# Kernel optimization log

Measured on AMD Instinct MI355X. Metric: run time of the kernel, lower is better.

The kernel has to match this reference:

```python
import jax, jax.numpy as jnp
import numpy as np

N, E, H, L, B = 50000, 1250000, 64, 64, 500
BN_EPS = 1e-5


def _bn(x, g, b):
    # training-mode BatchNorm1d: per-feature batch mean / biased var
    m = jnp.mean(x, axis=0)
    v = jnp.mean((x - m) ** 2, axis=0)
    return (x - m) * jax.lax.rsqrt(v + BN_EPS) * g + b


def _gconv(h, edge_attr, src, dst):
    # message: softplus(x_j + edge_attr); aggr='add'; eps=0 -> + (1+0)*h
    msg = jax.nn.softplus(h[src] + edge_attr)          # [E,H]
    agg = jax.ops.segment_sum(msg, dst, num_segments=N)  # [N,H]
    return agg + h


def setup_inputs() -> dict:
    key = jax.random.key(0)
    ks = jax.random.split(key, 24)
    s = 0.05
    inp = {
        "x": jax.random.normal(ks[0], (E, 1), jnp.float32),
        "node_type": jax.random.randint(ks[1], (N,), 0, 100),
        "edge_type": jax.random.randint(ks[2], (E,), 0, 100),
        "edge_index": jax.random.randint(ks[3], (2, E), 0, N),
        "batch": jnp.sort(jax.random.randint(ks[4], (N,), 0, B)),
        "node_emb": jax.random.normal(ks[5], (100, H)) * s,
        "edge_emb": jax.random.normal(ks[6], (100, H)) * s,
        "w_d1": jax.random.normal(ks[7], (H, 1)) * s,
        "b_d1": jnp.zeros((H,)),
        "g_d1": jnp.ones((H,)), "be_d1": jnp.zeros((H,)),
        "w_d2": jax.random.normal(ks[8], (H, H)) * s,
        "b_d2": jnp.zeros((H,)),
        "g_d2": jnp.ones((H,)), "be_d2": jnp.zeros((H,)),
        "g_c1": jnp.ones((H,)), "be_c1": jnp.zeros((H,)),
        "g_c2": jnp.ones((H,)), "be_c2": jnp.zeros((H,)),
        "g_c3": jnp.ones((H,)), "be_c3": jnp.zeros((H,)),
        "w_o1": jax.random.normal(ks[9], (H, 2 * H)) * s,
        "b_o1": jnp.zeros((H,)),
        "g_o1": jnp.ones((H,)), "be_o1": jnp.zeros((H,)),
        "w_o2": jax.random.normal(ks[10], (H // 2, H)) * s,
        "b_o2": jnp.zeros((H // 2,)),
        "g_o2": jnp.ones((H // 2,)), "be_o2": jnp.zeros((H // 2,)),
        "w_o3": jax.random.normal(ks[11], (2 * L, H // 2)) * s,
        "b_o3": jnp.zeros((2 * L,)),
    }
    return inp


def reference(x, node_type, edge_type, edge_index, batch,
              node_emb, edge_emb,
              w_d1, b_d1, g_d1, be_d1,
              w_d2, b_d2, g_d2, be_d2,
              g_c1, be_c1, g_c2, be_c2, g_c3, be_c3,
              w_o1, b_o1, g_o1, be_o1,
              w_o2, b_o2, g_o2, be_o2,
              w_o3, b_o3):
    act = jax.nn.softplus
    src, dst = edge_index[0], edge_index[1]
    node_attr = node_emb[node_type]                    # [N,H]
    ea = edge_emb[edge_type]                           # [E,H]
    d = act(_bn(x @ w_d1.T + b_d1, g_d1, be_d1))       # [E,H]
    d = _bn(d @ w_d2.T + b_d2, g_d2, be_d2)
    ea = d * ea
    h = node_attr
    h = act(_bn(_gconv(h, ea, src, dst), g_c1, be_c1))
    h = act(_bn(_gconv(h, ea, src, dst), g_c2, be_c2))
    h = _bn(_gconv(h, ea, src, dst), g_c3, be_c3)
    h_global = jax.ops.segment_sum(h, batch, num_segments=B)  # [B,H]
    nf = jnp.concatenate([h, h_global[batch]], axis=-1)       # [N,2H]
    nf = act(_bn(nf @ w_o1.T + b_o1, g_o1, be_o1))
    nf = act(_bn(nf @ w_o2.T + b_o2, g_o2, be_o2))
    out = nf @ w_o3.T + b_o3                           # [N,2L]
    return out[:, :L], out[:, L:]
```

## Files before the change

### kernel.cpp

```cpp
#include <hip/hip_runtime.h>
#include <stdint.h>

#define NN 50000
#define EE 1250000
#define BB 500
#define BN_EPS 1e-5f
#define LOG2E 1.44269504f
#define LN2 0.69314718f

#define NBKT 391
#define NPBSH 7
#define NB1 256
#define BPB 4883

#define HBLK 88
#define HEPB ((EE + HBLK - 1) / HBLK)
#define FHSC 65536.f
#define FHIN (1.f / 65536.f)

#define NSL 16

#define NTB 8192
#define XLO (-12.0f)
#define XHI (12.0f)
#define XSC ((float)NTB / (XHI - XLO))
#define DXT ((XHI - XLO) / (float)NTB)
#define TPMAX 8191.999f

using u16 = unsigned short;
using u32 = unsigned int;

__device__ __forceinline__ u16 f2bf(float f) {
    u32 u = __float_as_uint(f);
    return (u16)((u + 0x7fffu + ((u >> 16) & 1u)) >> 16);
}
__device__ __forceinline__ u32 pk2(float a, float b) { return (u32)f2bf(a) | ((u32)f2bf(b) << 16); }
__device__ __forceinline__ float sp(float z) {
    float t = __builtin_amdgcn_exp2f(-fabsf(z) * LOG2E);
    float l = __builtin_amdgcn_logf(1.f + t) * LN2;
    return fmaxf(z, 0.f) + l;
}
__device__ __forceinline__ float rl(float v, int l) {
    return __uint_as_float(__builtin_amdgcn_readlane(__float_as_uint(v), l));
}

constexpr size_t OFF_ESD  = 0;
constexpr size_t OFF_ROWP = OFF_ESD + (size_t)EE * 16;
constexpr size_t OFF_HA   = (OFF_ROWP + (size_t)(NN + 1) * 4 + 255) & ~(size_t)255;
constexpr size_t OFF_HB   = OFF_HA + (size_t)NN * 64 * 4;
constexpr size_t OFF_ZB   = OFF_HB + (size_t)NN * 64 * 4;
constexpr size_t OFF_TMAT = OFF_ZB;
constexpr size_t OFF_TOT  = OFF_TMAT + (size_t)NB1 * NBKT * 4;
constexpr size_t OFF_BBASE= OFF_TOT + (size_t)NBKT * 4;
constexpr size_t OFF_YTAB = OFF_ZB + (size_t)NN * 32 * 4;
constexpr size_t OFF_PTAB = OFF_YTAB + (size_t)(NTB + 1) * 64 * 4;
constexpr size_t OFF_W2T  = OFF_PTAB + (size_t)NTB * 64 * 4;
constexpr size_t OFF_B2F  = OFF_W2T + 4096 * 4;
constexpr size_t OFF_W1T  = OFF_B2F + 256;
constexpr size_t OFF_W2O  = OFF_W1T + 8192 * 4;
constexpr size_t OFF_W3T  = OFF_W2O + 2048 * 4;
constexpr size_t OFF_BPTR = OFF_W3T + 4096 * 4;
constexpr size_t OFF_HG   = (OFF_BPTR + (BB + 1) * 4 + 255) & ~(size_t)255;
constexpr size_t OFF_XSTAT= OFF_HG + (size_t)BB * 64 * 4;
constexpr size_t OFF_STY  = OFF_XSTAT + 16;
constexpr size_t OFF_FST  = OFF_STY + 128 * 8;
constexpr size_t ZERO_END = OFF_FST + 5 * NSL * 128 * 4;
constexpr size_t ZERO_BYTES = ZERO_END - OFF_HG;
constexpr size_t OFF_HPART= (ZERO_END + 255) & ~(size_t)255;

__global__ void __launch_bounds__(256) k_prep0(
        const float* __restrict__ w2, const float* __restrict__ b2,
        const float* __restrict__ w1, const float* __restrict__ wo2, const float* __restrict__ w3,
        const float* __restrict__ x, const int* __restrict__ batch, const int* __restrict__ dstv,
        float* __restrict__ w2T, float* __restrict__ b2f,
        float* __restrict__ w1T, float* __restrict__ w2T2, float* __restrict__ w3T,
        double* __restrict__ xstat, int* __restrict__ bptr, int* __restrict__ T) {
    int bx = blockIdx.x, t = threadIdx.x;
    if (bx < 16) {
        int idx = bx * 256 + t;
        int hin = idx >> 6, ho = idx & 63;
        w2T[idx] = w2[ho * 64 + hin];
        if (idx < 64) b2f[idx] = b2[idx];
    } else if (bx < 72) {
        int idx = (bx - 16) * 256 + t;
        if (idx < 8192) {
            int j = idx >> 6, ho = idx & 63;
            w1T[idx] = w1[ho * 128 + j];
        } else if (idx < 8192 + 2048) {
            int q = idx - 8192;
            int j = q >> 5, ho = q & 31;
            w2T2[q] = wo2[ho * 64 + j];
        } else if (idx < 8192 + 2048 + 4096) {
            int q = idx - 8192 - 2048;
            int j = q >> 7, jo = q & 127;
            w3T[q] = w3[jo * 32 + j];
        }
    } else if (bx < 584) {
        __shared__ float ls[256], lq[256];
        float s = 0, q = 0;
        for (int i = (bx - 72) * 256 + t; i < EE; i += 512 * 256) {
            float v = x[i]; s += v; q += v * v;
        }
        ls[t] = s; lq[t] = q; __syncthreads();
        for (int off = 128; off > 0; off >>= 1) {
            if (t < off) { ls[t] += ls[t + off]; lq[t] += lq[t + off]; }
            __syncthreads();
        }
        if (t == 0) { atomicAdd(&xstat[0], (double)ls[0]); atomicAdd(&xstat[1], (double)lq[0]); }
    } else if (bx < 780) {
        int n = (bx - 584) * 256 + t;
        if (n >= NN) return;
        int b = batch[n];
        int pb = (n == 0) ? -1 : batch[n - 1];
        for (int k = pb + 1; k <= b; k++) bptr[k] = n;
        if (n == NN - 1) { for (int k = b + 1; k <= BB; k++) bptr[k] = NN; }
    } else {
        __shared__ int hh[NBKT];
        for (int i = t; i < NBKT; i += 256) hh[i] = 0;
        __syncthreads();
        int bb = bx - 780;
        int e0 = bb * BPB;
        int e1 = e0 + BPB; if (e1 > EE) e1 = EE;
        for (int e = e0 + t; e < e1; e += 256)
            atomicAdd(&hh[dstv[e] >> NPBSH], 1);
        __syncthreads();
        for (int i = t; i < NBKT; i += 256)
            T[(size_t)bb * NBKT + i] = hh[i];
    }
}

__global__ void k_bscanA(int* __restrict__ T, int* __restrict__ tot) {
    __shared__ int ls[256];
    int b = blockIdx.x, t = threadIdx.x;
    int v = T[(size_t)t * NBKT + b];
    ls[t] = v; __syncthreads();
    for (int off = 1; off < 256; off <<= 1) {
        int a = ls[t]; int add = (t >= off) ? ls[t - off] : 0; __syncthreads();
        ls[t] = a + add; __syncthreads();
    }
    T[(size_t)t * NBKT + b] = ls[t] - v;
    if (t == 255) tot[b] = ls[255];
}

__global__ void __launch_bounds__(1024) k_binhist(
        const float* __restrict__ x, const int* __restrict__ src,
        const int* __restrict__ dstv, const int* __restrict__ etv,
        const int* __restrict__ T, const int* __restrict__ tot,
        int* __restrict__ bbase_g, int4* __restrict__ esd_tmp, int* __restrict__ hpart) {
    __shared__ int shb[3 * (NTB / 2)];
    int t = threadIdx.x;
    if (blockIdx.x < NB1) {
        int* cur = shb;
        int* sls = shb + 512;
        int v = 0;
        if (t < 512) { v = (t < NBKT) ? tot[t] : 0; sls[t] = v; }
        __syncthreads();
        for (int off = 1; off < 512; off <<= 1) {
            int a = 0;
            if (t < 512) { a = sls[t]; if (t >= off) a += sls[t - off]; }
            __syncthreads();
            if (t < 512) sls[t] = a;
            __syncthreads();
        }
        if (t < NBKT) {
            int base = sls[t] - v;
            cur[t] = base + T[(size_t)blockIdx.x * NBKT + t];
            if (blockIdx.x == 0) bbase_g[t] = base;
        }
        if (blockIdx.x == 0 && t == 0) bbase_g[NBKT] = EE;
        __syncthreads();
        int e0 = blockIdx.x * BPB;
        int e1 = e0 + BPB; if (e1 > EE) e1 = EE;
        for (int e = e0 + t; e < e1; e += 1024) {
            int d = dstv[e];
            int p = atomicAdd(&cur[d >> NPBSH], 1);
            float tp = fminf(fmaxf((x[e] - XLO) * XSC, 0.f), TPMAX);
            int i = (int)tp; float f = tp - (float)i;
            int4 vv; vv.x = src[e]; vv.y = etv[e] | ((d & 127) << 7); vv.z = i; vv.w = __float_as_int(f);
            esd_tmp[p] = vv;
        }
    } else {
        int* cnt = shb; int* sf = shb + NTB / 2; int* sf2 = shb + NTB;
        int bb = blockIdx.x - NB1;
        int e0 = bb * HEPB;
        int e1 = e0 + HEPB; if (e1 > EE) e1 = EE;
        int* outp = hpart + (size_t)bb * 3 * NTB;
        for (int half = 0; half < 2; half++) {
            for (int i = t; i < NTB / 2; i += 1024) { cnt[i] = 0; sf[i] = 0; sf2[i] = 0; }
            __syncthreads();
            int lo = half * (NTB / 2);
            for (int e = e0 + t; e < e1; e += 1024) {
                float tp = fminf(fmaxf((x[e] - XLO) * XSC, 0.f), TPMAX);
                int i = (int)tp;
                int li = i - lo;
                if ((unsigned)li < (unsigned)(NTB / 2)) {
                    float f = tp - (float)i;
                    atomicAdd(&cnt[li], 1);
                    atomicAdd(&sf[li], (int)(f * FHSC));
                    atomicAdd(&sf2[li], (int)(f * f * FHSC));
                }
            }
            __syncthreads();
            for (int i = t; i < NTB / 2; i += 1024) {
                outp[lo + i] = cnt[i];
                outp[NTB + lo + i] = sf[i];
                outp[2 * NTB + lo + i] = sf2[i];
            }
            __syncthreads();
        }
    }
}

__global__ void __launch_bounds__(256) k_locyt(
        const int4* __restrict__ esd_tmp, const int* __restrict__ bbase,
        int* __restrict__ row_ptr, int4* __restrict__ esd,
        const double* __restrict__ xstat, const float* __restrict__ w_d1,
        const float* __restrict__ g_d1, const float* __restrict__ be_d1,
        const float* __restrict__ w2T, const float* __restrict__ b2f,
        const int* __restrict__ hpart, float* __restrict__ ytab, double* __restrict__ sty) {
    __shared__ char shraw[65 * 64 * 4 + 192 * 4];
    int t = threadIdx.x;
    if (blockIdx.x < NBKT) {
        int* hist = (int*)shraw;
        int* ls   = hist + 128;
        int* cur  = ls + 128;
        int b = blockIdx.x;
        if (b == 0 && t == 0) row_ptr[NN] = EE;
        int base = bbase[b], end = bbase[b + 1];
        if (t < 128) hist[t] = 0;
        __syncthreads();
        for (int p = base + t; p < end; p += 256)
            atomicAdd(&hist[(esd_tmp[p].y >> 7) & 127], 1);
        __syncthreads();
        int v = 0;
        if (t < 128) { v = hist[t]; ls[t] = v; }
        __syncthreads();
        for (int off = 1; off < 128; off <<= 1) {
            int a = 0;
            if (t < 128) { a = ls[t]; if (t >= off) a += ls[t - off]; }
            __syncthreads();
            if (t < 128) ls[t] = a;
            __syncthreads();
        }
        if (t < 128) {
            int exc = ls[t] - v;
            cur[t] = base + exc;
            int n = (b << NPBSH) + t;
            if (n < NN) row_ptr[n] = base + exc;
        }
        __syncthreads();
        for (int p = base + t; p < end; p += 256) {
            int4 r = esd_tmp[p];
            int ld = (r.y >> 7) & 127;
            r.y &= 127;
            esd[atomicAdd(&cur[ld], 1)] = r;
        }
    } else {
        float (*kn)[64] = (float(*)[64])shraw;
        float* hs = (float*)(shraw + 65 * 64 * 4);
        int lane = t & 63, w = t >> 6;
        int g = blockIdx.x - NBKT;
        double inv = 1.0 / (double)EE;
        double mx = xstat[0] * inv;
        double vx = xstat[1] * inv - mx * mx; if (vx < 0) vx = 0;
        float wd = w_d1[lane];
        float Aw = wd * rsqrtf((float)vx * wd * wd + BN_EPS) * g_d1[lane];
        float Cw = be_d1[lane];
        for (int kk = w; kk < 65; kk += 4) {
            int idx = (g << 6) + kk;
            float xi = XLO + (float)idx * DXT;
            float tt = xi - (float)mx;
            float d1L = sp(fmaf(Aw, tt, Cw));
            float y = b2f[lane];
            #pragma unroll
            for (int hin = 0; hin < 64; hin++)
                y = fmaf(rl(d1L, hin), w2T[hin * 64 + lane], y);
            kn[kk][lane] = y;
            if (kk < 64 || g == 127) ytab[(idx << 6) | lane] = y;
        }
        if (t < 192) {
            int slot = t >> 6, ii = t & 63;
            float s = 0.f;
            size_t off = (size_t)slot * NTB + (g << 6) + ii;
            for (int b = 0; b < HBLK; b++)
                s += (float)hpart[(size_t)b * 3 * NTB + off];
            hs[t] = (slot == 0) ? s : s * FHIN;
        }
        __syncthreads();
        if (t >= 64) return;
        double S = 0.0, Q = 0.0;
        float aprev = kn[0][lane];
        for (int ii = 0; ii < 64; ii++) {
            float c = hs[ii], f1 = hs[64 + ii], f2 = hs[128 + ii];
            float b = kn[ii + 1][lane];
            float a = aprev; aprev = b;
            float d = b - a;
            S += (double)(fmaf(c, a, d * f1));
            Q += (double)(fmaf(c * a, a, fmaf(2.f * a * d, f1, d * d * f2)));
        }
        atomicAdd(&sty[lane], S);
        atomicAdd(&sty[64 + lane], Q);
    }
}

__global__ void k_ypack(const float* __restrict__ ytab, const double* __restrict__ sty,
                        const float* __restrict__ g2, const float* __restrict__ be2,
                        u32* __restrict__ ptab) {
    int tid = blockIdx.x * 256 + threadIdx.x;
    int f = tid & 63;
    double inv = 1.0 / (double)EE;
    double m = sty[f] * inv;
    double var = sty[64 + f] * inv - m * m; if (var < 0) var = 0;
    float rstd = rsqrtf((float)var + BN_EPS);
    float sc0 = rstd * g2[f];
    float sc = sc0 * LOG2E;
    float sh = (be2[f] - (float)m * sc0) * LOG2E;
    float a = fmaf(ytab[tid], sc, sh);
    float b = fmaf(ytab[tid + 64], sc, sh);
    ptab[tid] = pk2(a, b - a);
}

__device__ __forceinline__ float edge_term(int4 ed, int lane, const u32* __restrict__ ptab,
                                           const float* __restrict__ emb) {
    u32 pr = ptab[(ed.z << 6) | lane];
    float f = __int_as_float(ed.w);
    float a = __uint_as_float(pr << 16);
    float d = __uint_as_float(pr & 0xffff0000u);
    float y = fmaf(f, d, a);
    return y * emb[(ed.y << 6) | lane];
}
__device__ __forceinline__ void sp2(float hv, float av, float& accm, float& accl) {
    float z = fmaf(hv, LOG2E, av);
    float t = __builtin_amdgcn_exp2f(-fabsf(z));
    accm += fmaxf(z, 0.f);
    accl += __builtin_amdgcn_logf(1.f + t);
}

__global__ void __launch_bounds__(128) k_agg(
        const float* __restrict__ h, const int4* __restrict__ esd, const int* __restrict__ row_ptr,
        const u32* __restrict__ ptab, const float* __restrict__ emb, float* __restrict__ hpre) {
    int lane = threadIdx.x & 63;
    int n = __builtin_amdgcn_readfirstlane((int)((blockIdx.x << 1) | (threadIdx.x >> 6)));
    int p0 = row_ptr[n], p1 = row_ptr[n + 1];
    float accm = 0.f, accl = 0.f;
    int p = p0;
    for (; p + 4 <= p1; p += 4) {
        int4 e0 = esd[p], e1 = esd[p + 1], e2 = esd[p + 2], e3 = esd[p + 3];
        float h0 = h[(e0.x << 6) | lane];
        float h1 = h[(e1.x << 6) | lane];
        float h2 = h[(e2.x << 6) | lane];
        float h3 = h[(e3.x << 6) | lane];
        float a0 = edge_term(e0, lane, ptab, emb);
        float a1 = edge_term(e1, lane, ptab, emb);
        float a2 = edge_term(e2, lane, ptab, emb);
        float a3 = edge_term(e3, lane, ptab, emb);
        sp2(h0, a0, accm, accl);
        sp2(h1, a1, accm, accl);
        sp2(h2, a2, accm, accl);
        sp2(h3, a3, accm, accl);
    }
    for (; p < p1; ++p) {
        int4 e0 = esd[p];
        float h0 = h[(e0.x << 6) | lane];
        sp2(h0, edge_term(e0, lane, ptab, emb), accm, accl);
    }
    int o = (n << 6) | lane;
    hpre[o] = fmaf(accm + accl, LN2, h[o]);
}

__global__ void __launch_bounds__(128) k_agg0(
        const int* __restrict__ nt, const float* __restrict__ nemb, const int4* __restrict__ esd,
        const int* __restrict__ row_ptr, const u32* __restrict__ ptab,
        const float* __restrict__ emb, float* __restrict__ hpre) {
    int lane = threadIdx.x & 63;
    int n = __builtin_amdgcn_readfirstlane((int)((blockIdx.x << 1) | (threadIdx.x >> 6)));
    int p0 = row_ptr[n], p1 = row_ptr[n + 1];
    float accm = 0.f, accl = 0.f;
    int p = p0;
    for (; p + 4 <= p1; p += 4) {
        int4 e0 = esd[p], e1 = esd[p + 1], e2 = esd[p + 2], e3 = esd[p + 3];
        float h0 = nemb[(nt[e0.x] << 6) | lane];
        float h1 = nemb[(nt[e1.x] << 6) | lane];
        float h2 = nemb[(nt[e2.x] << 6) | lane];
        float h3 = nemb[(nt[e3.x] << 6) | lane];
        float a0 = edge_term(e0, lane, ptab, emb);
        float a1 = edge_term(e1, lane, ptab, emb);
        float a2 = edge_term(e2, lane, ptab, emb);
        float a3 = edge_term(e3, lane, ptab, emb);
        sp2(h0, a0, accm, accl);
        sp2(h1, a1, accm, accl);
        sp2(h2, a2, accm, accl);
        sp2(h3, a3, accm, accl);
    }
    for (; p < p1; ++p) {
        int4 e0 = esd[p];
        float h0 = nemb[(nt[e0.x] << 6) | lane];
        sp2(h0, edge_term(e0, lane, ptab, emb), accm, accl);
    }
    hpre[(n << 6) | lane] = fmaf(accm + accl, LN2, nemb[(nt[n] << 6) | lane]);
}

__global__ void __launch_bounds__(256) k_fstats(
        const float* __restrict__ v, int rows, float* __restrict__ stat) {
    int f = threadIdx.x & 63;
    int r0 = threadIdx.x >> 6;
    float s = 0.f, q = 0.f;
    for (int r = blockIdx.x * 4 + r0; r < rows; r += gridDim.x * 4) {
        float val = v[(size_t)r * 64 + f];
        s += val; q += val * val;
    }
    __shared__ float lsS[4][64], lsQ[4][64];
    lsS[r0][f] = s; lsQ[r0][f] = q; __syncthreads();
    if (threadIdx.x < 128) {
        int ff = threadIdx.x & 63; bool isq = threadIdx.x >= 64;
        float r = 0.f;
        #pragma unroll
        for (int j = 0; j < 4; j++) r += isq ? lsQ[j][ff] : lsS[j][ff];
        int sl = ((int)blockIdx.x & (NSL - 1)) << 7;
        unsafeAtomicAdd(&stat[sl + (isq ? 64 : 0) + ff], r);
    }
}

__global__ void __launch_bounds__(256) k_bn(
        const float* __restrict__ in, float* __restrict__ out,
        const float* __restrict__ stat, const float* __restrict__ g,
        const float* __restrict__ be, int rows, int logC, int act) {
    int C = 1 << logC;
    __shared__ float scl[64], shl[64];
    int t = threadIdx.x;
    if (t < C) {
        float s = 0.f, q = 0.f;
        #pragma unroll
        for (int sl = 0; sl < NSL; sl++) {
            s += stat[(sl << 7) + t];
            q += stat[(sl << 7) + 64 + t];
        }
        float inv = 1.f / (float)rows;
        float m = s * inv;
        float var = q * inv - m * m; if (var < 0.f) var = 0.f;
        float rstd = rsqrtf(var + BN_EPS);
        float sc = rstd * g[t];
        scl[t] = sc; shl[t] = be[t] - m * sc;
    }
    __syncthreads();
    size_t total = (size_t)rows << logC;
    size_t i = (size_t)blockIdx.x * 256 + t;
    if (i >= total) return;
    int f = (int)(i & (C - 1));
    float val = fmaf(in[i], scl[f], shl[f]);
    out[i] = act ? sp(val) : val;
}

__global__ void __launch_bounds__(256) k_hg2(
        const float* __restrict__ h, const int* __restrict__ bptr, float* __restrict__ hg) {
    int b = blockIdx.x;
    int lane = threadIdx.x & 63, w = threadIdx.x >> 6;
    int n0 = bptr[b], n1 = bptr[b + 1];
    float acc = 0.f;
    for (int n = n0 + w; n < n1; n += 4)
        acc += h[(n << 6) | lane];
    __shared__ float ls[256];
    ls[threadIdx.x] = acc; __syncthreads();
    if (threadIdx.x < 64)
        hg[(b << 6) | lane] = ls[lane] + ls[64 + lane] + ls[128 + lane] + ls[192 + lane];
}

#define O1NPW 4
__global__ void __launch_bounds__(256) k_o1(
        const float* __restrict__ h, const float* __restrict__ hg, const int* __restrict__ batch,
        const float* __restrict__ w1T, const float* __restrict__ b1, float* __restrict__ z1,
        float* __restrict__ stat) {
    int lane = threadIdx.x & 63;
    int wv = (blockIdx.x * 256 + (int)threadIdx.x) >> 6;
    int n0 = __builtin_amdgcn_readfirstlane(wv * O1NPW);
    float hl[O1NPW], gl[O1NPW], acc[O1NPW];
    float bl = b1[lane];
    #pragma unroll
    for (int k = 0; k < O1NPW; k++) {
        int n = n0 + k;
        hl[k] = h[(n << 6) | lane];
        gl[k] = hg[(batch[n] << 6) | lane];
        acc[k] = bl;
    }
    #pragma unroll
    for (int j = 0; j < 64; j++) {
        float w = w1T[(j << 6) | lane];
        #pragma unroll
        for (int k = 0; k < O1NPW; k++)
            acc[k] = fmaf(rl(hl[k], j), w, acc[k]);
    }
    #pragma unroll
    for (int j = 0; j < 64; j++) {
        float w = w1T[((64 + j) << 6) | lane];
        #pragma unroll
        for (int k = 0; k < O1NPW; k++)
            acc[k] = fmaf(rl(gl[k], j), w, acc[k]);
    }
    float s = 0.f, q = 0.f;
    #pragma unroll
    for (int k = 0; k < O1NPW; k++) {
        z1[((n0 + k) << 6) | lane] = acc[k];
        s += acc[k]; q += acc[k] * acc[k];
    }
    __shared__ float lsS[4][64], lsQ[4][64];
    int w = threadIdx.x >> 6;
    lsS[w][lane] = s; lsQ[w][lane] = q; __syncthreads();
    if (threadIdx.x < 128) {
        int f = threadIdx.x & 63; bool isq = threadIdx.x >= 64;
        float r = 0.f;
        #pragma unroll
        for (int j = 0; j < 4; j++) r += isq ? lsQ[j][f] : lsS[j][f];
        int sl = ((int)blockIdx.x & (NSL - 1)) << 7;
        unsafeAtomicAdd(&stat[sl + (isq ? 64 : 0) + f], r);
    }
}

__global__ void __launch_bounds__(256) k_o2(
        const float* __restrict__ o1v, const float* __restrict__ w2T2,
        const float* __restrict__ b2, float* __restrict__ z2, float* __restrict__ stat) {
    int lane = threadIdx.x & 63;
    int ho = lane & 31;
    int wv = (blockIdx.x * 256 + (int)threadIdx.x) >> 6;
    int n0 = __builtin_amdgcn_readfirstlane(wv * 8);
    float xr[8], acc[4];
    #pragma unroll
    for (int k = 0; k < 8; k++) {
        int n = n0 + k; if (n >= NN) n = NN - 1;
        xr[k] = o1v[(n << 6) | lane];
    }
    float bl = b2[ho];
    #pragma unroll
    for (int k = 0; k < 4; k++) acc[k] = bl;
    #pragma unroll
    for (int j = 0; j < 64; j++) {
        float w = w2T2[(j << 5) | ho];
        #pragma unroll
        for (int k = 0; k < 4; k++) {
            float slo = rl(xr[k], j);
            float shi = rl(xr[4 + k], j);
            float v = (lane < 32) ? slo : shi;
            acc[k] = fmaf(v, w, acc[k]);
        }
    }
    int nbase = n0 + ((lane >> 5) << 2);
    float s = 0.f, q = 0.f;
    #pragma unroll
    for (int k = 0; k < 4; k++) {
        if (nbase + k < NN) {
            z2[((nbase + k) << 5) | ho] = acc[k];
            s += acc[k]; q += acc[k] * acc[k];
        }
    }
    __shared__ float lsS[4][64], lsQ[4][64];
    int w = threadIdx.x >> 6;
    lsS[w][lane] = s; lsQ[w][lane] = q; __syncthreads();
    if (threadIdx.x < 64) {
        int f = threadIdx.x & 31; bool isq = threadIdx.x >= 32;
        float r = 0.f;
        #pragma unroll
        for (int j = 0; j < 4; j++)
            r += isq ? (lsQ[j][f] + lsQ[j][32 + f]) : (lsS[j][f] + lsS[j][32 + f]);
        int sl = ((int)blockIdx.x & (NSL - 1)) << 7;
        unsafeAtomicAdd(&stat[sl + (isq ? 64 : 0) + f], r);
    }
}

__global__ void __launch_bounds__(256) k_o3(
        const float* __restrict__ o2v, const float* __restrict__ w3T,
        const float* __restrict__ b3, float* __restrict__ outp) {
    int lane = threadIdx.x & 63;
    int wv = (blockIdx.x * 256 + (int)threadIdx.x) >> 6;
    int n0 = __builtin_amdgcn_readfirstlane((wv >> 1) << 2);
    int jo = (((wv & 1) << 6) + lane);
    if (n0 >= NN) return;
    float zl[4], acc[4];
    float bl = b3[jo];
    #pragma unroll
    for (int k = 0; k < 4; k++) {
        zl[k] = o2v[((n0 + k) << 5) | (lane & 31)];
        acc[k] = bl;
    }
    #pragma unroll
    for (int j = 0; j < 32; j++) {
        float w = w3T[(j << 7) | jo];
        #pragma unroll
        for (int k = 0; k < 4; k++)
            acc[k] = fmaf(rl(zl[k], j), w, acc[k]);
    }
    #pragma unroll
    for (int k = 0; k < 4; k++) {
        int n = n0 + k;
        size_t dsti = (jo < 64) ? ((size_t)(n << 6) + jo)
                                : ((size_t)NN * 64 + (size_t)(n << 6) + (jo - 64));
        outp[dsti] = acc[k];
    }
}

extern "C" void kernel_launch(void* const* d_in, const int* in_sizes, int n_in,
                              void* d_out, int out_size, void* d_ws, size_t ws_size,
                              hipStream_t stream) {
    const float* x        = (const float*)d_in[0];
    const int* node_type  = (const int*)d_in[1];
    const int* edge_type  = (const int*)d_in[2];
    const int* edge_index = (const int*)d_in[3];
    const int* batch      = (const int*)d_in[4];
    const float* node_emb = (const float*)d_in[5];
    const float* edge_emb = (const float*)d_in[6];
    const float* w_d1 = (const float*)d_in[7];  const float* b_d1 = (const float*)d_in[8];
    const float* g_d1 = (const float*)d_in[9];  const float* be_d1 = (const float*)d_in[10];
    const float* w_d2 = (const float*)d_in[11]; const float* b_d2 = (const float*)d_in[12];
    const float* g_d2 = (const float*)d_in[13]; const float* be_d2 = (const float*)d_in[14];
    const float* g_c1 = (const float*)d_in[15]; const float* be_c1 = (const float*)d_in[16];
    const float* g_c2 = (const float*)d_in[17]; const float* be_c2 = (const float*)d_in[18];
    const float* g_c3 = (const float*)d_in[19]; const float* be_c3 = (const float*)d_in[20];
    const float* w_o1 = (const float*)d_in[21]; const float* b_o1 = (const float*)d_in[22];
    const float* g_o1 = (const float*)d_in[23]; const float* be_o1 = (const float*)d_in[24];
    const float* w_o2 = (const float*)d_in[25]; const float* b_o2 = (const float*)d_in[26];
    const float* g_o2 = (const float*)d_in[27]; const float* be_o2 = (const float*)d_in[28];
    const float* w_o3 = (const float*)d_in[29]; const float* b_o3 = (const float*)d_in[30];
    (void)b_d1;
    const int* src  = edge_index;
    const int* dstv = edge_index + EE;

    char* ws = (char*)d_ws;
    int4*  esd     = (int4*)(ws + OFF_ESD);
    int*   row_ptr = (int*)(ws + OFF_ROWP);
    float* hA   = (float*)(ws + OFF_HA);
    float* hB   = (float*)(ws + OFF_HB);
    float* zb   = (float*)(ws + OFF_ZB);
    int4*  esd_tmp = (int4*)(ws + OFF_HA);
    int*   hpart = (int*)(ws + OFF_HPART);
    int*   T    = (int*)(ws + OFF_TMAT);
    int*   tot  = (int*)(ws + OFF_TOT);
    int*   bbase= (int*)(ws + OFF_BBASE);
    float* ytab = (float*)(ws + OFF_YTAB);
    u32*   ptab = (u32*)(ws + OFF_PTAB);
    float* w2T  = (float*)(ws + OFF_W2T);
    float* b2f  = (float*)(ws + OFF_B2F);
    float* w1T  = (float*)(ws + OFF_W1T);
    float* w2T2 = (float*)(ws + OFF_W2O);
    float* w3T  = (float*)(ws + OFF_W3T);
    int*   bptr = (int*)(ws + OFF_BPTR);
    float* hg     = (float*)(ws + OFF_HG);
    double* xstat = (double*)(ws + OFF_XSTAT);
    double* sty   = (double*)(ws + OFF_STY);
    float* fst    = (float*)(ws + OFF_FST);
    float* st0 = fst;               float* st1 = fst + NSL * 128;
    float* st2 = fst + 2 * NSL * 128;
    float* st3 = fst + 3 * NSL * 128;
    float* st4 = fst + 4 * NSL * 128;

    hipMemsetAsync(ws + OFF_HG, 0, ZERO_BYTES, stream);

    k_prep0<<<1036, 256, 0, stream>>>(w_d2, b_d2, w_o1, w_o2, w_o3, x, batch, dstv,
                                      w2T, b2f, w1T, w2T2, w3T, xstat, bptr, T);
    k_bscanA<<<NBKT, 256, 0, stream>>>(T, tot);
    k_binhist<<<NB1 + HBLK, 1024, 0, stream>>>(x, src, dstv, edge_type, T, tot,
                                               bbase, esd_tmp, hpart);
    k_locyt<<<NBKT + 128, 256, 0, stream>>>(esd_tmp, bbase, row_ptr, esd,
                                            xstat, w_d1, g_d1, be_d1, w2T, b2f,
                                            hpart, ytab, sty);
    k_ypack<<<NTB * 64 / 256, 256, 0, stream>>>(ytab, sty, g_d2, be_d2, ptab);
    k_agg0<<<25000, 128, 0, stream>>>(node_type, node_emb, esd, row_ptr, ptab, edge_emb, hB);
    k_fstats<<<1024, 256, 0, stream>>>(hB, NN, st0);
    k_bn<<<12500, 256, 0, stream>>>(hB, hB, st0, g_c1, be_c1, NN, 6, 1);
    k_agg<<<25000, 128, 0, stream>>>(hB, esd, row_ptr, ptab, edge_emb, hA);
    k_fstats<<<1024, 256, 0, stream>>>(hA, NN, st1);
    k_bn<<<12500, 256, 0, stream>>>(hA, hA, st1, g_c2, be_c2, NN, 6, 1);
    k_agg<<<25000, 128, 0, stream>>>(hA, esd, row_ptr, ptab, edge_emb, hB);
    k_fstats<<<1024, 256, 0, stream>>>(hB, NN, st2);
    k_bn<<<12500, 256, 0, stream>>>(hB, hB, st2, g_c3, be_c3, NN, 6, 0);
    k_hg2<<<BB, 256, 0, stream>>>(hB, bptr, hg);
    k_o1<<<3125, 256, 0, stream>>>(hB, hg, batch, w1T, b_o1, hA, st3);
    k_bn<<<12500, 256, 0, stream>>>(hA, hA, st3, g_o1, be_o1, NN, 6, 1);
    k_o2<<<1563, 256, 0, stream>>>(hA, w2T2, b_o2, zb, st4);
    k_bn<<<6250, 256, 0, stream>>>(zb, zb, st4, g_o2, be_o2, NN, 5, 1);
    k_o3<<<6250, 256, 0, stream>>>(zb, w3T, b_o3, (float*)d_out);
    (void)in_sizes; (void)n_in; (void)out_size; (void)ws_size;
}
```

Before: 508.4 us.

## Fuse graph-sum into last BN, materialize initial node features, drop agg0 and bptr

Removes the k_hg2 per-graph reduction by having the final BatchNorm kernel atomically add each output into the per-graph sum, and drops the batch-pointer construction from the prep kernel. The specialized first aggregation kernel, which gathered node embeddings through node_type indirection for every edge, is replaced: k_ypack now writes the initial node features into a buffer, and the generic k_agg runs on it. Double atomics are switched to unsafeAtomicAdd. The exchange is 3.2M float atomics onto 32K addresses, with heavy contention because batch is sorted, plus an extra write and read of the initial feature buffer.

```diff
diff --git a/kernel.cpp b/kernel.cpp
--- a/kernel.cpp
+++ b/kernel.cpp
@@ -71,10 +71,10 @@
 __global__ void __launch_bounds__(256) k_prep0(
         const float* __restrict__ w2, const float* __restrict__ b2,
         const float* __restrict__ w1, const float* __restrict__ wo2, const float* __restrict__ w3,
-        const float* __restrict__ x, const int* __restrict__ batch, const int* __restrict__ dstv,
+        const float* __restrict__ x, const int* __restrict__ dstv,
         float* __restrict__ w2T, float* __restrict__ b2f,
         float* __restrict__ w1T, float* __restrict__ w2T2, float* __restrict__ w3T,
-        double* __restrict__ xstat, int* __restrict__ bptr, int* __restrict__ T) {
+        double* __restrict__ xstat, int* __restrict__ T) {
     int bx = blockIdx.x, t = threadIdx.x;
     if (bx < 16) {
         int idx = bx * 256 + t;
@@ -106,19 +106,12 @@
             if (t < off) { ls[t] += ls[t + off]; lq[t] += lq[t + off]; }
             __syncthreads();
         }
-        if (t == 0) { atomicAdd(&xstat[0], (double)ls[0]); atomicAdd(&xstat[1], (double)lq[0]); }
-    } else if (bx < 780) {
-        int n = (bx - 584) * 256 + t;
-        if (n >= NN) return;
-        int b = batch[n];
-        int pb = (n == 0) ? -1 : batch[n - 1];
-        for (int k = pb + 1; k <= b; k++) bptr[k] = n;
-        if (n == NN - 1) { for (int k = b + 1; k <= BB; k++) bptr[k] = NN; }
+        if (t == 0) { unsafeAtomicAdd(&xstat[0], (double)ls[0]); unsafeAtomicAdd(&xstat[1], (double)lq[0]); }
     } else {
         __shared__ int hh[NBKT];
         for (int i = t; i < NBKT; i += 256) hh[i] = 0;
         __syncthreads();
-        int bb = bx - 780;
+        int bb = bx - 584;
         int e0 = bb * BPB;
         int e1 = e0 + BPB; if (e1 > EE) e1 = EE;
         for (int e = e0 + t; e < e1; e += 256)
@@ -298,14 +291,16 @@
             S += (double)(fmaf(c, a, d * f1));
             Q += (double)(fmaf(c * a, a, fmaf(2.f * a * d, f1, d * d * f2)));
         }
-        atomicAdd(&sty[lane], S);
-        atomicAdd(&sty[64 + lane], Q);
+        unsafeAtomicAdd(&sty[lane], S);
+        unsafeAtomicAdd(&sty[64 + lane], Q);
     }
 }
 
 __global__ void k_ypack(const float* __restrict__ ytab, const double* __restrict__ sty,
                         const float* __restrict__ g2, const float* __restrict__ be2,
-                        u32* __restrict__ ptab) {
+                        u32* __restrict__ ptab,
+                        const int* __restrict__ nt, const float* __restrict__ nemb,
+                        float* __restrict__ h0) {
     int tid = blockIdx.x * 256 + threadIdx.x;
     int f = tid & 63;
     double inv = 1.0 / (double)EE;
@@ -318,6 +313,10 @@
     float a = fmaf(ytab[tid], sc, sh);
     float b = fmaf(ytab[tid + 64], sc, sh);
     ptab[tid] = pk2(a, b - a);
+    for (size_t i = tid; i < (size_t)NN * 64; i += (size_t)NTB * 64) {
+        int n = (int)(i >> 6);
+        h0[i] = nemb[(nt[n] << 6) | ((int)i & 63)];
+    }
 }
 
 __device__ __forceinline__ float edge_term(int4 ed, int lane, const u32* __restrict__ ptab,
@@ -368,38 +367,6 @@
     hpre[o] = fmaf(accm + accl, LN2, h[o]);
 }
 
-__global__ void __launch_bounds__(128) k_agg0(
-        const int* __restrict__ nt, const float* __restrict__ nemb, const int4* __restrict__ esd,
-        const int* __restrict__ row_ptr, const u32* __restrict__ ptab,
-        const float* __restrict__ emb, float* __restrict__ hpre) {
-    int lane = threadIdx.x & 63;
-    int n = __builtin_amdgcn_readfirstlane((int)((blockIdx.x << 1) | (threadIdx.x >> 6)));
-    int p0 = row_ptr[n], p1 = row_ptr[n + 1];
-    float accm = 0.f, accl = 0.f;
-    int p = p0;
-    for (; p + 4 <= p1; p += 4) {
-        int4 e0 = esd[p], e1 = esd[p + 1], e2 = esd[p + 2], e3 = esd[p + 3];
-        float h0 = nemb[(nt[e0.x] << 6) | lane];
-        float h1 = nemb[(nt[e1.x] << 6) | lane];
-        float h2 = nemb[(nt[e2.x] << 6) | lane];
-        float h3 = nemb[(nt[e3.x] << 6) | lane];
-        float a0 = edge_term(e0, lane, ptab, emb);
-        float a1 = edge_term(e1, lane, ptab, emb);
-        float a2 = edge_term(e2, lane, ptab, emb);
-        float a3 = edge_term(e3, lane, ptab, emb);
-        sp2(h0, a0, accm, accl);
-        sp2(h1, a1, accm, accl);
-        sp2(h2, a2, accm, accl);
-        sp2(h3, a3, accm, accl);
-    }
-    for (; p < p1; ++p) {
-        int4 e0 = esd[p];
-        float h0 = nemb[(nt[e0.x] << 6) | lane];
-        sp2(h0, edge_term(e0, lane, ptab, emb), accm, accl);
-    }
-    hpre[(n << 6) | lane] = fmaf(accm + accl, LN2, nemb[(nt[n] << 6) | lane]);
-}
-
 __global__ void __launch_bounds__(256) k_fstats(
         const float* __restrict__ v, int rows, float* __restrict__ stat) {
     int f = threadIdx.x & 63;
@@ -424,7 +391,8 @@
 __global__ void __launch_bounds__(256) k_bn(
         const float* __restrict__ in, float* __restrict__ out,
         const float* __restrict__ stat, const float* __restrict__ g,
-        const float* __restrict__ be, int rows, int logC, int act) {
+        const float* __restrict__ be, int rows, int logC, int act,
+        float* __restrict__ hgOpt, const int* __restrict__ batch) {
     int C = 1 << logC;
     __shared__ float scl[64], shl[64];
     int t = threadIdx.x;
@@ -448,21 +416,12 @@
     if (i >= total) return;
     int f = (int)(i & (C - 1));
     float val = fmaf(in[i], scl[f], shl[f]);
-    out[i] = act ? sp(val) : val;
-}
-
-__global__ void __launch_bounds__(256) k_hg2(
-        const float* __restrict__ h, const int* __restrict__ bptr, float* __restrict__ hg) {
-    int b = blockIdx.x;
-    int lane = threadIdx.x & 63, w = threadIdx.x >> 6;
-    int n0 = bptr[b], n1 = bptr[b + 1];
-    float acc = 0.f;
-    for (int n = n0 + w; n < n1; n += 4)
-        acc += h[(n << 6) | lane];
-    __shared__ float ls[256];
-    ls[threadIdx.x] = acc; __syncthreads();
-    if (threadIdx.x < 64)
-        hg[(b << 6) | lane] = ls[lane] + ls[64 + lane] + ls[128 + lane] + ls[192 + lane];
+    float ov = act ? sp(val) : val;
+    out[i] = ov;
+    if (hgOpt) {
+        int n = (int)(i >> logC);
+        unsafeAtomicAdd(&hgOpt[(batch[n] << 6) | f], ov);
+    }
 }
 
 #define O1NPW 4
@@ -640,7 +599,6 @@
     float* w1T  = (float*)(ws + OFF_W1T);
     float* w2T2 = (float*)(ws + OFF_W2O);
     float* w3T  = (float*)(ws + OFF_W3T);
-    int*   bptr = (int*)(ws + OFF_BPTR);
     float* hg     = (float*)(ws + OFF_HG);
     double* xstat = (double*)(ws + OFF_XSTAT);
     double* sty   = (double*)(ws + OFF_STY);
@@ -652,29 +610,29 @@
 
     hipMemsetAsync(ws + OFF_HG, 0, ZERO_BYTES, stream);
 
-    k_prep0<<<1036, 256, 0, stream>>>(w_d2, b_d2, w_o1, w_o2, w_o3, x, batch, dstv,
-                                      w2T, b2f, w1T, w2T2, w3T, xstat, bptr, T);
+    k_prep0<<<840, 256, 0, stream>>>(w_d2, b_d2, w_o1, w_o2, w_o3, x, dstv,
+                                     w2T, b2f, w1T, w2T2, w3T, xstat, T);
     k_bscanA<<<NBKT, 256, 0, stream>>>(T, tot);
     k_binhist<<<NB1 + HBLK, 1024, 0, stream>>>(x, src, dstv, edge_type, T, tot,
                                                bbase, esd_tmp, hpart);
     k_locyt<<<NBKT + 128, 256, 0, stream>>>(esd_tmp, bbase, row_ptr, esd,
                                             xstat, w_d1, g_d1, be_d1, w2T, b2f,
                                             hpart, ytab, sty);
-    k_ypack<<<NTB * 64 / 256, 256, 0, stream>>>(ytab, sty, g_d2, be_d2, ptab);
-    k_agg0<<<25000, 128, 0, stream>>>(node_type, node_emb, esd, row_ptr, ptab, edge_emb, hB);
+    k_ypack<<<NTB * 64 / 256, 256, 0, stream>>>(ytab, sty, g_d2, be_d2, ptab,
+                                                node_type, node_emb, hA);
+    k_agg<<<25000, 128, 0, stream>>>(hA, esd, row_ptr, ptab, edge_emb, hB);
     k_fstats<<<1024, 256, 0, stream>>>(hB, NN, st0);
-    k_bn<<<12500, 256, 0, stream>>>(hB, hB, st0, g_c1, be_c1, NN, 6, 1);
+    k_bn<<<12500, 256, 0, stream>>>(hB, hB, st0, g_c1, be_c1, NN, 6, 1, nullptr, nullptr);
     k_agg<<<25000, 128, 0, stream>>>(hB, esd, row_ptr, ptab, edge_emb, hA);
     k_fstats<<<1024, 256, 0, stream>>>(hA, NN, st1);
-    k_bn<<<12500, 256, 0, stream>>>(hA, hA, st1, g_c2, be_c2, NN, 6, 1);
+    k_bn<<<12500, 256, 0, stream>>>(hA, hA, st1, g_c2, be_c2, NN, 6, 1, nullptr, nullptr);
     k_agg<<<25000, 128, 0, stream>>>(hA, esd, row_ptr, ptab, edge_emb, hB);
     k_fstats<<<1024, 256, 0, stream>>>(hB, NN, st2);
-    k_bn<<<12500, 256, 0, stream>>>(hB, hB, st2, g_c3, be_c3, NN, 6, 0);
-    k_hg2<<<BB, 256, 0, stream>>>(hB, bptr, hg);
+    k_bn<<<12500, 256, 0, stream>>>(hB, hB, st2, g_c3, be_c3, NN, 6, 0, hg, batch);
     k_o1<<<3125, 256, 0, stream>>>(hB, hg, batch, w1T, b_o1, hA, st3);
-    k_bn<<<12500, 256, 0, stream>>>(hA, hA, st3, g_o1, be_o1, NN, 6, 1);
+    k_bn<<<12500, 256, 0, stream>>>(hA, hA, st3, g_o1, be_o1, NN, 6, 1, nullptr, nullptr);
     k_o2<<<1563, 256, 0, stream>>>(hA, w2T2, b_o2, zb, st4);
-    k_bn<<<6250, 256, 0, stream>>>(zb, zb, st4, g_o2, be_o2, NN, 5, 1);
+    k_bn<<<6250, 256, 0, stream>>>(zb, zb, st4, g_o2, be_o2, NN, 5, 1, nullptr, nullptr);
     k_o3<<<6250, 256, 0, stream>>>(zb, w3T, b_o3, (float*)d_out);
     (void)in_sizes; (void)n_in; (void)out_size; (void)ws_size;
 }
```

Measured after the change: 522.7 us. 2.8% more time.
